# Performance work log

Measured on AMD Instinct MI355X. Metric: run time of the kernel, lower is better.

## Reference

```python
import jax, jax.numpy as jnp
import numpy as np

N = 100000   # nodes
E = 1600000  # edges (before self-loops)
F = 128      # num_features
H = 128      # hidden_dim
EPS = 1e-5   # BatchNorm eps


def setup_inputs() -> dict:
    key = jax.random.key(0)
    ks = jax.random.split(key, 8)
    x = jax.random.normal(ks[0], (N, F), dtype=jnp.float32)
    edge_index = jax.random.randint(ks[1], (2, E), 0, N, dtype=jnp.int64)

    def lin(k, din, dout):
        s = 1.0 / np.sqrt(din)
        kw, kb = jax.random.split(k)
        W = jax.random.uniform(kw, (din, dout), jnp.float32, -s, s)
        b = jax.random.uniform(kb, (dout,), jnp.float32, -s, s)
        return W, b

    W1, b1 = lin(ks[2], F, H)
    W2, b2 = lin(ks[3], H, H)
    W3, b3 = lin(ks[4], H, H)
    Wc, bc = lin(ks[5], H, 2)

    def bn_params():
        return (jnp.ones((H,), jnp.float32), jnp.zeros((H,), jnp.float32),
                jnp.zeros((H,), jnp.float32), jnp.ones((H,), jnp.float32))

    g1, be1, rm1, rv1 = bn_params()
    g2, be2, rm2, rv2 = bn_params()
    g3, be3, rm3, rv3 = bn_params()

    return {"x": x, "edge_index": edge_index,
            "W1": W1, "b1": b1, "W2": W2, "b2": b2, "W3": W3, "b3": b3,
            "g1": g1, "be1": be1, "rm1": rm1, "rv1": rv1,
            "g2": g2, "be2": be2, "rm2": rm2, "rv2": rv2,
            "g3": g3, "be3": be3, "rm3": rm3, "rv3": rv3,
            "Wc": Wc, "bc": bc}


def _gcn_norm(edge_index, num_nodes):
    # add self-loops, compute symmetric normalization (PyG GCNConv default)
    loop = jnp.arange(num_nodes, dtype=edge_index.dtype)
    src = jnp.concatenate([edge_index[0], loop])
    dst = jnp.concatenate([edge_index[1], loop])
    deg = jax.ops.segment_sum(jnp.ones_like(dst, dtype=jnp.float32), dst,
                              num_segments=num_nodes)
    dinv = jnp.where(deg > 0, jax.lax.rsqrt(deg), 0.0)
    norm = dinv[src] * dinv[dst]  # [E+N]
    return src, dst, norm


def _gcn_conv(x, W, b, src, dst, norm, num_nodes):
    h = x @ W                              # [N, H] linear first
    msg = h[src] * norm[:, None]           # gather + scale  [E+N, H]
    out = jax.ops.segment_sum(msg, dst, num_segments=num_nodes)  # scatter-add
    return out + b


def _bn_eval(x, g, be, rm, rv):
    return (x - rm) * jax.lax.rsqrt(rv + EPS) * g + be


def reference(x, edge_index,
              W1, b1, W2, b2, W3, b3,
              g1, be1, rm1, rv1,
              g2, be2, rm2, rv2,
              g3, be3, rm3, rv3,
              Wc, bc):
    n = x.shape[0]
    src, dst, norm = _gcn_norm(edge_index, n)
    h = _gcn_conv(x, W1, b1, src, dst, norm, n)
    h = _bn_eval(jax.nn.relu(h), g1, be1, rm1, rv1)
    # dropout: identity in eval mode
    h = _gcn_conv(h, W2, b2, src, dst, norm, n)
    h = _bn_eval(jax.nn.relu(h), g2, be2, rm2, rv2)
    h = _gcn_conv(h, W3, b3, src, dst, norm, n)
    h = _bn_eval(jax.nn.relu(h), g3, be3, rm3, rv3)
    return h @ Wc + bc  # [N, 2]
```

## Files before the change

kernel.cpp:

```cpp
#include <hip/hip_runtime.h>
#include <hip/hip_fp16.h>

#define BN_EPS 1e-5f
#define CHUNK 4096
#define BBITS 7

typedef _Float16 half8 __attribute__((ext_vector_type(8)));
typedef float f32x4 __attribute__((ext_vector_type(4)));

__device__ __forceinline__ float4 f4zero() { return make_float4(0.f, 0.f, 0.f, 0.f); }


__global__ __launch_bounds__(256) void k_pack_hist(const float* __restrict__ W1,
                                                   const float* __restrict__ W2,
                                                   const float* __restrict__ W3,
                                                   _Float16* __restrict__ pW,
                                                   const int* __restrict__ dst,
                                                   int* __restrict__ tableT,
                                                   int nA, int nbuck, int e) {
    __shared__ int h[1024];
    int tid = threadIdx.x;
    if (blockIdx.x < 24) {
        int t = blockIdx.x * 256 + tid;
        int wi = t >> 11;
        int tt = t & 2047;
        const float* W = (wi == 0) ? W1 : ((wi == 1) ? W2 : W3);
        int kc = tt >> 9;
        int rem = tt & 511;
        int ct = rem >> 6;
        int lane = rem & 63;
        int q = lane >> 4;
        int col = ct * 16 + (lane & 15);
        half8 hh;
#pragma unroll
        for (int j = 0; j < 8; ++j)
            hh[j] = (_Float16)W[(kc * 32 + q * 8 + j) * 128 + col];
        *(half8*)(pW + (size_t)t * 8) = hh;
        return;
    }
    int blk = blockIdx.x - 24;
    for (int k = tid; k < 1024; k += 256) h[k] = 0;
    __syncthreads();
    int base = blk * CHUNK;
    if (base + CHUNK <= e && (e & 3) == 0) {
        const int4* d4 = (const int4*)(dst + base);
#pragma unroll
        for (int t = 0; t < CHUNK / 1024; ++t) {
            int4 d = d4[t * 256 + tid];
            atomicAdd(&h[d.x >> BBITS], 1);
            atomicAdd(&h[d.y >> BBITS], 1);
            atomicAdd(&h[d.z >> BBITS], 1);
            atomicAdd(&h[d.w >> BBITS], 1);
        }
    } else {
        for (int i = base + tid; i < e && i < base + CHUNK; i += 256)
            atomicAdd(&h[dst[i] >> BBITS], 1);
    }
    __syncthreads();
    for (int k = tid; k < nbuck; k += 256)
        tableT[(size_t)k * nA + blk] = h[k];
}


__global__ __launch_bounds__(1024) void k_scan_block(const int* __restrict__ in,
                                                     int* __restrict__ outp,
                                                     int* __restrict__ partials, int len) {
    __shared__ int s[1024];
    int t = threadIdx.x;
    int gid = blockIdx.x * 1024 + t;
    int v = (gid < len) ? in[gid] : 0;
    int x = v;
    s[t] = x;
    __syncthreads();
    for (int d = 1; d < 1024; d <<= 1) {
        int y = (t >= d) ? s[t - d] : 0;
        __syncthreads();
        x += y;
        s[t] = x;
        __syncthreads();
    }
    if (gid < len) outp[gid] = x - v;
    if (t == 1023) partials[blockIdx.x] = x;
}

__global__ __launch_bounds__(256) void k_scan_addp(int* __restrict__ data,
                                                   const int* __restrict__ partials, int len) {
    __shared__ int red[256];
    int tid = threadIdx.x;
    int K = blockIdx.x >> 2;
    int s = 0;
    for (int t = tid; t < K; t += 256) s += partials[t];
    red[tid] = s;
    __syncthreads();
    for (int d = 128; d > 0; d >>= 1) {
        if (tid < d) red[tid] += red[tid + d];
        __syncthreads();
    }
    int gid = blockIdx.x * 256 + tid;
    if (gid < len) data[gid] += red[0];
}


__global__ __launch_bounds__(256) void k_bucket_scatter(const int* __restrict__ src,
                                                        const int* __restrict__ dst,
                                                        const int* __restrict__ tableT,
                                                        int2* __restrict__ bed,
                                                        int nA, int nbuck, int e) {
    __shared__ int cur[1024];
    int blk = blockIdx.x, tid = threadIdx.x;
    for (int k = tid; k < nbuck; k += 256)
        cur[k] = tableT[(size_t)k * nA + blk];
    __syncthreads();
    int base = blk * CHUNK;
    if (base + CHUNK <= e && (e & 3) == 0) {
        const int4* s4 = (const int4*)(src + base);
        const int4* d4 = (const int4*)(dst + base);
#pragma unroll
        for (int t = 0; t < CHUNK / 1024; ++t) {
            int4 s = s4[t * 256 + tid];
            int4 d = d4[t * 256 + tid];
            int p0 = atomicAdd(&cur[d.x >> BBITS], 1); bed[p0] = make_int2(s.x, d.x);
            int p1 = atomicAdd(&cur[d.y >> BBITS], 1); bed[p1] = make_int2(s.y, d.y);
            int p2 = atomicAdd(&cur[d.z >> BBITS], 1); bed[p2] = make_int2(s.z, d.z);
            int p3 = atomicAdd(&cur[d.w >> BBITS], 1); bed[p3] = make_int2(s.w, d.w);
        }
    } else {
        for (int i = base + tid; i < e && i < base + CHUNK; i += 256) {
            int d = dst[i];
            int p = atomicAdd(&cur[d >> BBITS], 1);
            bed[p] = make_int2(src[i], d);
        }
    }
}


__global__ __launch_bounds__(256) void k_bucket_rank(const int2* __restrict__ bed,
                                                     const int* __restrict__ tableT,
                                                     int* __restrict__ brank,
                                                     int* __restrict__ counts,
                                                     float* __restrict__ dinv,
                                                     int* __restrict__ localOff,
                                                     int* __restrict__ btot,
                                                     int nA, int nbuck, int n, int e) {
    __shared__ int lcnt[128];
    __shared__ int lscan[128];
    int b = blockIdx.x, tid = threadIdx.x;
    if (tid < 128) lcnt[tid] = 0;
    __syncthreads();
    int start = tableT[(size_t)b * nA];
    int end = (b + 1 < nbuck) ? tableT[(size_t)(b + 1) * nA] : e;
    for (int i = start + tid; i < end; i += 256) {
        int2 q = bed[i];
        brank[i] = atomicAdd(&lcnt[q.y & 127], 1);
    }
    __syncthreads();
    int padded = 0;
    if (tid < 128) {
        padded = (lcnt[tid] + 7) & ~7;
        lscan[tid] = padded;
    }
    __syncthreads();
    for (int d = 1; d < 128; d <<= 1) {
        int y = (tid < 128 && tid >= d) ? lscan[tid - d] : 0;
        __syncthreads();
        if (tid < 128) lscan[tid] += y;
        __syncthreads();
    }
    if (tid < 128) {
        int node = (b << BBITS) + tid;
        if (node < n) {
            int c = lcnt[tid];
            counts[node] = c;
            dinv[node] = rsqrtf((float)(c + 1));
            localOff[node] = lscan[tid] - padded;
        }
        if (tid == 127) btot[b] = lscan[127];
    }
}


__global__ __launch_bounds__(1024) void k_scan_buckets(const int* __restrict__ btot,
                                                       int* __restrict__ bucketBase, int nbuck) {
    __shared__ int s[1024];
    int t = threadIdx.x;
    int v = (t < nbuck) ? btot[t] : 0;
    int x = v;
    s[t] = x;
    __syncthreads();
    for (int d = 1; d < 1024; d <<= 1) {
        int y = (t >= d) ? s[t - d] : 0;
        __syncthreads();
        x += y;
        s[t] = x;
        __syncthreads();
    }
    if (t < nbuck) bucketBase[t] = x - v;
    if (t == nbuck - 1) bucketBase[nbuck] = x;
}


__global__ __launch_bounds__(256) void k_finalize(const int* __restrict__ counts,
                                                  const int* __restrict__ localOff,
                                                  const int* __restrict__ bucketBase,
                                                  int* __restrict__ offs,
                                                  int* __restrict__ er,
                                                  const int2* __restrict__ bed,
                                                  const int* __restrict__ brank,
                                                  unsigned int* __restrict__ bufAzero,
                                                  int n, int e, int gN, int nbuck) {
    int tid = threadIdx.x;
    if (blockIdx.x < gN) {
        int node = blockIdx.x * 256 + tid;
        if (node < n) {
            int c = counts[node];
            int o = bucketBase[node >> BBITS] + localOff[node];
            offs[node] = o;
            int pc = (c + 7) & ~7;
            for (int j = c; j < pc; ++j) er[o + j] = n;
        }
        if (node == 0) offs[n] = bucketBase[nbuck];
        if (blockIdx.x == 0 && tid < 64) bufAzero[tid] = 0u;
    } else {
        int i = ((blockIdx.x - gN) * 256 + tid) * 2;
        if (i + 1 < e) {
            int4 q = *(const int4*)(bed + i);
            int2 r = *(const int2*)(brank + i);
            er[bucketBase[q.y >> BBITS] + localOff[q.y] + r.x] = q.x;
            er[bucketBase[q.w >> BBITS] + localOff[q.w] + r.y] = q.z;
        } else if (i < e) {
            int2 q = bed[i];
            er[bucketBase[q.y >> BBITS] + localOff[q.y] + brank[i]] = q.x;
        }
    }
}


template <bool AF32>
__global__ __launch_bounds__(256) void k_gemm_mfma(const void* __restrict__ Av,
                                                   const _Float16* __restrict__ pW,
                                                   const float* __restrict__ dinv,
                                                   uint4* __restrict__ C, int n) {
    __shared__ char smem[32768];
    uint4* sW = (uint4*)smem;
    int tid = threadIdx.x;

    {
        const uint4* gW = (const uint4*)pW;
#pragma unroll
        for (int i = 0; i < 8; ++i) sW[tid + 256 * i] = gW[tid + 256 * i];
    }
    __syncthreads();

    int wave = tid >> 6, lane = tid & 63;
    int quad = lane >> 4, l16 = lane & 15;
    int row0 = blockIdx.x * 64 + wave * 16;
    int arow = row0 + l16;
    int arowc = (arow < n) ? arow : (n - 1);

    half8 af[4];
    if (AF32) {
        const float* A = (const float*)Av + (size_t)arowc * 128 + quad * 8;
#pragma unroll
        for (int kc = 0; kc < 4; ++kc) {
            float4 lo = *(const float4*)(A + kc * 32);
            float4 hi = *(const float4*)(A + kc * 32 + 4);
            half8 h;
            h[0] = (_Float16)lo.x; h[1] = (_Float16)lo.y;
            h[2] = (_Float16)lo.z; h[3] = (_Float16)lo.w;
            h[4] = (_Float16)hi.x; h[5] = (_Float16)hi.y;
            h[6] = (_Float16)hi.z; h[7] = (_Float16)hi.w;
            af[kc] = h;
        }
    } else {
        const _Float16* A = (const _Float16*)Av + (size_t)arowc * 128 + quad * 8;
#pragma unroll
        for (int kc = 0; kc < 4; ++kc)
            af[kc] = *(const half8*)(A + kc * 32);
    }

    f32x4 acc[8];
#pragma unroll
    for (int ct = 0; ct < 8; ++ct) acc[ct] = (f32x4){0.f, 0.f, 0.f, 0.f};

#pragma unroll
    for (int kc = 0; kc < 4; ++kc) {
#pragma unroll
        for (int ct = 0; ct < 8; ++ct) {
            half8 bf = *(half8*)&sW[(kc * 8 + ct) * 64 + lane];
            acc[ct] = __builtin_amdgcn_mfma_f32_16x16x32_f16(af[kc], bf, acc[ct], 0, 0, 0);
        }
    }

    __syncthreads();

    _Float16* eb = (_Float16*)smem + wave * 16 * 136;
    float dv[4];
#pragma unroll
    for (int r = 0; r < 4; ++r) {
        int rr = row0 + quad * 4 + r;
        dv[r] = dinv[(rr < n) ? rr : (n - 1)];
    }
#pragma unroll
    for (int ct = 0; ct < 8; ++ct)
#pragma unroll
        for (int r = 0; r < 4; ++r)
            eb[(quad * 4 + r) * 136 + ct * 16 + l16] = (_Float16)(acc[ct][r] * dv[r]);

#pragma unroll
    for (int i = 0; i < 4; ++i) {
        int linear = i * 64 + lane;
        int r = linear >> 4, c = linear & 15;
        uint4 v = *(uint4*)((char*)eb + r * 272 + c * 16);
        int row = row0 + r;
        if (row < n) C[(size_t)row * 16 + c] = v;
    }
}


__device__ __forceinline__ void acc_row(float4& acc, uint2 q) {
    float2 f01 = __half22float2(*(__half2*)&q.x);
    float2 f23 = __half22float2(*(__half2*)&q.y);
    acc.x += f01.x; acc.y += f01.y; acc.z += f23.x; acc.w += f23.y;
}

template <bool FUSE_CLS>
__global__ __launch_bounds__(256) void k_aggregate(const uint2* __restrict__ Ah,
                                                   const int* __restrict__ offs,
                                                   const int* __restrict__ er,
                                                   const float* __restrict__ dinv,
                                                   const float* __restrict__ bias,
                                                   const float* __restrict__ g,
                                                   const float* __restrict__ be,
                                                   const float* __restrict__ rm,
                                                   const float* __restrict__ rv,
                                                   uint2* __restrict__ Hout,
                                                   const float* __restrict__ Wc,
                                                   const float* __restrict__ bc,
                                                   float* __restrict__ out, int n) {
    int lane = threadIdx.x & 31;
    int node = blockIdx.x * 8 + (threadIdx.x >> 5);
    if (node >= n) return;

    float4 acc = f4zero();
    acc_row(acc, Ah[(size_t)node * 32 + lane]);

    int e0 = offs[node], e1 = offs[node + 1];
    for (int e = e0; e < e1; e += 8) {
        int4 ra = *(const int4*)(er + e);
        int4 rb = *(const int4*)(er + e + 4);
        uint2 v0 = Ah[(size_t)ra.x * 32 + lane];
        uint2 v1 = Ah[(size_t)ra.y * 32 + lane];
        uint2 v2 = Ah[(size_t)ra.z * 32 + lane];
        uint2 v3 = Ah[(size_t)ra.w * 32 + lane];
        uint2 v4 = Ah[(size_t)rb.x * 32 + lane];
        uint2 v5 = Ah[(size_t)rb.y * 32 + lane];
        uint2 v6 = Ah[(size_t)rb.z * 32 + lane];
        uint2 v7 = Ah[(size_t)rb.w * 32 + lane];
        acc_row(acc, v0); acc_row(acc, v1); acc_row(acc, v2); acc_row(acc, v3);
        acc_row(acc, v4); acc_row(acc, v5); acc_row(acc, v6); acc_row(acc, v7);
    }

    float di = dinv[node];
    acc.x *= di; acc.y *= di; acc.z *= di; acc.w *= di;

    float4 b4  = ((const float4*)bias)[lane];
    float4 g4  = ((const float4*)g)[lane];
    float4 be4 = ((const float4*)be)[lane];
    float4 rm4 = ((const float4*)rm)[lane];
    float4 rv4 = ((const float4*)rv)[lane];

    float4 o;
    float v;
    v = fmaxf(acc.x + b4.x, 0.f); o.x = (v - rm4.x) * rsqrtf(rv4.x + BN_EPS) * g4.x + be4.x;
    v = fmaxf(acc.y + b4.y, 0.f); o.y = (v - rm4.y) * rsqrtf(rv4.y + BN_EPS) * g4.y + be4.y;
    v = fmaxf(acc.z + b4.z, 0.f); o.z = (v - rm4.z) * rsqrtf(rv4.z + BN_EPS) * g4.z + be4.z;
    v = fmaxf(acc.w + b4.w, 0.f); o.w = (v - rm4.w) * rsqrtf(rv4.w + BN_EPS) * g4.w + be4.w;

    if (!FUSE_CLS) {
        __half2 p0 = __floats2half2_rn(o.x, o.y);
        __half2 p1 = __floats2half2_rn(o.z, o.w);
        uint2 u;
        u.x = *(unsigned int*)&p0;
        u.y = *(unsigned int*)&p1;
        Hout[(size_t)node * 32 + lane] = u;
    } else {
        const float4* Wv = (const float4*)Wc;
        float4 w01 = Wv[2 * lane];
        float4 w23 = Wv[2 * lane + 1];
        float p0 = o.x * w01.x + o.y * w01.z + o.z * w23.x + o.w * w23.z;
        float p1 = o.x * w01.y + o.y * w01.w + o.z * w23.y + o.w * w23.w;
#pragma unroll
        for (int d = 16; d >= 1; d >>= 1) {
            p0 += __shfl_down(p0, d, 32);
            p1 += __shfl_down(p1, d, 32);
        }
        if (lane == 0) {
            out[node * 2 + 0] = p0 + bc[0];
            out[node * 2 + 1] = p1 + bc[1];
        }
    }
}


extern "C" void kernel_launch(void* const* d_in, const int* in_sizes, int n_in,
                              void* d_out, int out_size, void* d_ws, size_t ws_size,
                              hipStream_t stream) {
    const float* x   = (const float*)d_in[0];
    const int*   ei  = (const int*)d_in[1];
    const float* W1  = (const float*)d_in[2];
    const float* b1  = (const float*)d_in[3];
    const float* W2  = (const float*)d_in[4];
    const float* b2  = (const float*)d_in[5];
    const float* W3  = (const float*)d_in[6];
    const float* b3  = (const float*)d_in[7];
    const float* g1  = (const float*)d_in[8];
    const float* be1 = (const float*)d_in[9];
    const float* rm1 = (const float*)d_in[10];
    const float* rv1 = (const float*)d_in[11];
    const float* g2  = (const float*)d_in[12];
    const float* be2 = (const float*)d_in[13];
    const float* rm2 = (const float*)d_in[14];
    const float* rv2 = (const float*)d_in[15];
    const float* g3  = (const float*)d_in[16];
    const float* be3 = (const float*)d_in[17];
    const float* rm3 = (const float*)d_in[18];
    const float* rv3 = (const float*)d_in[19];
    const float* Wc  = (const float*)d_in[20];
    const float* bc  = (const float*)d_in[21];
    float* out = (float*)d_out;

    int n = in_sizes[0] / 128;
    int e = in_sizes[1] / 2;
    const int* src = ei;
    const int* dst = ei + e;

    char* ws = (char*)d_ws;
    size_t off = 0;
    auto alloc = [&](size_t bytes) -> char* {
        char* p = ws + off;
        off += (bytes + 255) & ~(size_t)255;
        return p;
    };
    int nA    = (e + CHUNK - 1) / CHUNK;
    int nbuck = (n + (1 << BBITS) - 1) >> BBITS;
    int tlen  = nbuck * nA;
    int erCap = e + 8 * n;

    char*      bufA     = (char*) alloc((size_t)(n + 1) * 256);
    char*      bufH     = (char*) alloc((size_t)n * 256);
    float*     dinv     = (float*)alloc((size_t)n * 4);
    int*       counts   = (int*)  alloc((size_t)n * 4);
    int*       offs     = (int*)  alloc((size_t)(n + 1) * 4);
    int*       localOff = (int*)  alloc((size_t)n * 4);
    int*       btot     = (int*)  alloc((size_t)(nbuck + 1) * 4);
    int*       bktBase  = (int*)  alloc((size_t)(nbuck + 1) * 4);
    int*       tableT   = (int*)  alloc((size_t)(tlen + 1) * 4);
    int*       parts    = (int*)  alloc(8192);
    int*       er       = (int*)  alloc((size_t)erCap * 4);
    _Float16*  pW       = (_Float16*)alloc(3 * 16384 * 2);
    (void)ws_size; (void)n_in; (void)out_size;

    int2* bed   = (int2*)bufH;
    int*  brank = (int*)(bufH + (size_t)e * 8);

    int gN  = (n + 255) / 256;
    int nbT = (tlen + 1023) / 1024;

    k_pack_hist<<<24 + nA, 256, 0, stream>>>(W1, W2, W3, pW, dst, tableT, nA, nbuck, e);
    k_scan_block<<<nbT, 1024, 0, stream>>>(tableT, tableT, parts, tlen);
    k_scan_addp<<<(tlen + 255) / 256, 256, 0, stream>>>(tableT, parts, tlen);
    k_bucket_scatter<<<nA, 256, 0, stream>>>(src, dst, tableT, bed, nA, nbuck, e);
    k_bucket_rank<<<nbuck, 256, 0, stream>>>(bed, tableT, brank, counts, dinv, localOff,
                                             btot, nA, nbuck, n, e);
    k_scan_buckets<<<1, 1024, 0, stream>>>(btot, bktBase, nbuck);
    int gP = gN + (e / 2 + 255) / 256 + 1;
    k_finalize<<<gP, 256, 0, stream>>>(counts, localOff, bktBase, offs, er, bed, brank,
                                       (unsigned int*)(bufA + (size_t)n * 256), n, e, gN, nbuck);

    int gGemm = (n + 63) / 64;
    int gAgg  = (n + 7) / 8;

    k_gemm_mfma<true><<<gGemm, 256, 0, stream>>>(x, pW, dinv, (uint4*)bufA, n);
    k_aggregate<false><<<gAgg, 256, 0, stream>>>((const uint2*)bufA, offs, er, dinv,
                                                 b1, g1, be1, rm1, rv1, (uint2*)bufH,
                                                 nullptr, nullptr, nullptr, n);

    k_gemm_mfma<false><<<gGemm, 256, 0, stream>>>(bufH, pW + 16384, dinv, (uint4*)bufA, n);
    k_aggregate<false><<<gAgg, 256, 0, stream>>>((const uint2*)bufA, offs, er, dinv,
                                                 b2, g2, be2, rm2, rv2, (uint2*)bufH,
                                                 nullptr, nullptr, nullptr, n);

    k_gemm_mfma<false><<<gGemm, 256, 0, stream>>>(bufH, pW + 32768, dinv, (uint4*)bufA, n);
    k_aggregate<true><<<gAgg, 256, 0, stream>>>((const uint2*)bufA, offs, er, dinv,
                                                b3, g3, be3, rm3, rv3, nullptr,
                                                Wc, bc, out, n);
}
```

Measured before the change: 394.7 us.

## Fuse CSR preprocessing kernels into one cooperative persistent kernel with grid syncs

Replaces seven separate preprocessing launches (weight pack and histogram, two-level scan, bucket scatter, bucket rank, bucket scan, finalize) with one cooperative kernel of 512 blocks that loops over work and separates phases with grid.sync. This is meant to remove launch gaps and tail effects between the small preprocessing kernels. The cost is that each phase is limited to a fixed grid with grid-stride loops, and each of the seven grid barriers adds its own overhead. The old alignment check ((e & 3) == 0) on the vectorized path is also dropped.

```diff
diff --git a/kernel.cpp b/kernel.cpp
--- a/kernel.cpp
+++ b/kernel.cpp
@@ -1,9 +1,13 @@
 #include <hip/hip_runtime.h>
 #include <hip/hip_fp16.h>
+#include <hip/hip_cooperative_groups.h>
+
+namespace cg = cooperative_groups;
 
 #define BN_EPS 1e-5f
 #define CHUNK 4096
 #define BBITS 7
+#define PREP_G 512
 
 typedef _Float16 half8 __attribute__((ext_vector_type(8)));
 typedef float f32x4 __attribute__((ext_vector_type(4)));
@@ -11,20 +15,35 @@
 __device__ __forceinline__ float4 f4zero() { return make_float4(0.f, 0.f, 0.f, 0.f); }
 
 
-__global__ __launch_bounds__(256) void k_pack_hist(const float* __restrict__ W1,
-                                                   const float* __restrict__ W2,
-                                                   const float* __restrict__ W3,
-                                                   _Float16* __restrict__ pW,
-                                                   const int* __restrict__ dst,
-                                                   int* __restrict__ tableT,
-                                                   int nA, int nbuck, int e) {
-    __shared__ int h[1024];
-    int tid = threadIdx.x;
-    if (blockIdx.x < 24) {
-        int t = blockIdx.x * 256 + tid;
+struct PrepArgs {
+    const float* W1; const float* W2; const float* W3;
+    _Float16* pW;
+    const int* src; const int* dst;
+    int* tableT;
+    int* parts;
+    int2* bed;
+    int* brank;
+    int* counts;
+    float* dinv;
+    int* localOff;
+    int* btot;
+    int* bucketBase;
+    int* offs;
+    int* er;
+    unsigned int* bufAzero;
+    int nA, nbuck, tlen, nseg, n, e;
+};
+
+__global__ __launch_bounds__(256) void k_prep(PrepArgs P) {
+    cg::grid_group grid = cg::this_grid();
+    __shared__ int smem[1280];
+    int bid = blockIdx.x, tid = threadIdx.x;
+    int G = gridDim.x;
+
+    for (int t = bid * 256 + tid; t < 6144; t += G * 256) {
         int wi = t >> 11;
         int tt = t & 2047;
-        const float* W = (wi == 0) ? W1 : ((wi == 1) ? W2 : W3);
+        const float* W = (wi == 0) ? P.W1 : ((wi == 1) ? P.W2 : P.W3);
         int kc = tt >> 9;
         int rem = tt & 511;
         int ct = rem >> 6;
@@ -35,201 +54,211 @@
 #pragma unroll
         for (int j = 0; j < 8; ++j)
             hh[j] = (_Float16)W[(kc * 32 + q * 8 + j) * 128 + col];
-        *(half8*)(pW + (size_t)t * 8) = hh;
-        return;
-    }
-    int blk = blockIdx.x - 24;
-    for (int k = tid; k < 1024; k += 256) h[k] = 0;
-    __syncthreads();
-    int base = blk * CHUNK;
-    if (base + CHUNK <= e && (e & 3) == 0) {
-        const int4* d4 = (const int4*)(dst + base);
-#pragma unroll
-        for (int t = 0; t < CHUNK / 1024; ++t) {
-            int4 d = d4[t * 256 + tid];
-            atomicAdd(&h[d.x >> BBITS], 1);
-            atomicAdd(&h[d.y >> BBITS], 1);
-            atomicAdd(&h[d.z >> BBITS], 1);
-            atomicAdd(&h[d.w >> BBITS], 1);
-        }
-    } else {
-        for (int i = base + tid; i < e && i < base + CHUNK; i += 256)
-            atomicAdd(&h[dst[i] >> BBITS], 1);
-    }
-    __syncthreads();
-    for (int k = tid; k < nbuck; k += 256)
-        tableT[(size_t)k * nA + blk] = h[k];
-}
-
-
-__global__ __launch_bounds__(1024) void k_scan_block(const int* __restrict__ in,
-                                                     int* __restrict__ outp,
-                                                     int* __restrict__ partials, int len) {
-    __shared__ int s[1024];
-    int t = threadIdx.x;
-    int gid = blockIdx.x * 1024 + t;
-    int v = (gid < len) ? in[gid] : 0;
-    int x = v;
-    s[t] = x;
-    __syncthreads();
-    for (int d = 1; d < 1024; d <<= 1) {
-        int y = (t >= d) ? s[t - d] : 0;
-        __syncthreads();
-        x += y;
-        s[t] = x;
-        __syncthreads();
-    }
-    if (gid < len) outp[gid] = x - v;
-    if (t == 1023) partials[blockIdx.x] = x;
-}
-
-__global__ __launch_bounds__(256) void k_scan_addp(int* __restrict__ data,
-                                                   const int* __restrict__ partials, int len) {
-    __shared__ int red[256];
-    int tid = threadIdx.x;
-    int K = blockIdx.x >> 2;
-    int s = 0;
-    for (int t = tid; t < K; t += 256) s += partials[t];
-    red[tid] = s;
-    __syncthreads();
-    for (int d = 128; d > 0; d >>= 1) {
-        if (tid < d) red[tid] += red[tid + d];
-        __syncthreads();
-    }
-    int gid = blockIdx.x * 256 + tid;
-    if (gid < len) data[gid] += red[0];
-}
-
-
-__global__ __launch_bounds__(256) void k_bucket_scatter(const int* __restrict__ src,
-                                                        const int* __restrict__ dst,
-                                                        const int* __restrict__ tableT,
-                                                        int2* __restrict__ bed,
-                                                        int nA, int nbuck, int e) {
-    __shared__ int cur[1024];
-    int blk = blockIdx.x, tid = threadIdx.x;
-    for (int k = tid; k < nbuck; k += 256)
-        cur[k] = tableT[(size_t)k * nA + blk];
-    __syncthreads();
-    int base = blk * CHUNK;
-    if (base + CHUNK <= e && (e & 3) == 0) {
-        const int4* s4 = (const int4*)(src + base);
-        const int4* d4 = (const int4*)(dst + base);
-#pragma unroll
-        for (int t = 0; t < CHUNK / 1024; ++t) {
-            int4 s = s4[t * 256 + tid];
-            int4 d = d4[t * 256 + tid];
-            int p0 = atomicAdd(&cur[d.x >> BBITS], 1); bed[p0] = make_int2(s.x, d.x);
-            int p1 = atomicAdd(&cur[d.y >> BBITS], 1); bed[p1] = make_int2(s.y, d.y);
-            int p2 = atomicAdd(&cur[d.z >> BBITS], 1); bed[p2] = make_int2(s.z, d.z);
-            int p3 = atomicAdd(&cur[d.w >> BBITS], 1); bed[p3] = make_int2(s.w, d.w);
-        }
-    } else {
-        for (int i = base + tid; i < e && i < base + CHUNK; i += 256) {
-            int d = dst[i];
-            int p = atomicAdd(&cur[d >> BBITS], 1);
-            bed[p] = make_int2(src[i], d);
-        }
-    }
-}
-
-
-__global__ __launch_bounds__(256) void k_bucket_rank(const int2* __restrict__ bed,
-                                                     const int* __restrict__ tableT,
-                                                     int* __restrict__ brank,
-                                                     int* __restrict__ counts,
-                                                     float* __restrict__ dinv,
-                                                     int* __restrict__ localOff,
-                                                     int* __restrict__ btot,
-                                                     int nA, int nbuck, int n, int e) {
-    __shared__ int lcnt[128];
-    __shared__ int lscan[128];
-    int b = blockIdx.x, tid = threadIdx.x;
-    if (tid < 128) lcnt[tid] = 0;
-    __syncthreads();
-    int start = tableT[(size_t)b * nA];
-    int end = (b + 1 < nbuck) ? tableT[(size_t)(b + 1) * nA] : e;
-    for (int i = start + tid; i < end; i += 256) {
-        int2 q = bed[i];
-        brank[i] = atomicAdd(&lcnt[q.y & 127], 1);
-    }
-    __syncthreads();
-    int padded = 0;
-    if (tid < 128) {
-        padded = (lcnt[tid] + 7) & ~7;
-        lscan[tid] = padded;
-    }
-    __syncthreads();
-    for (int d = 1; d < 128; d <<= 1) {
-        int y = (tid < 128 && tid >= d) ? lscan[tid - d] : 0;
-        __syncthreads();
-        if (tid < 128) lscan[tid] += y;
-        __syncthreads();
-    }
-    if (tid < 128) {
-        int node = (b << BBITS) + tid;
-        if (node < n) {
-            int c = lcnt[tid];
-            counts[node] = c;
-            dinv[node] = rsqrtf((float)(c + 1));
-            localOff[node] = lscan[tid] - padded;
-        }
-        if (tid == 127) btot[b] = lscan[127];
-    }
-}
-
-
-__global__ __launch_bounds__(1024) void k_scan_buckets(const int* __restrict__ btot,
-                                                       int* __restrict__ bucketBase, int nbuck) {
-    __shared__ int s[1024];
-    int t = threadIdx.x;
-    int v = (t < nbuck) ? btot[t] : 0;
-    int x = v;
-    s[t] = x;
-    __syncthreads();
-    for (int d = 1; d < 1024; d <<= 1) {
-        int y = (t >= d) ? s[t - d] : 0;
-        __syncthreads();
-        x += y;
-        s[t] = x;
-        __syncthreads();
-    }
-    if (t < nbuck) bucketBase[t] = x - v;
-    if (t == nbuck - 1) bucketBase[nbuck] = x;
-}
-
-
-__global__ __launch_bounds__(256) void k_finalize(const int* __restrict__ counts,
-                                                  const int* __restrict__ localOff,
-                                                  const int* __restrict__ bucketBase,
-                                                  int* __restrict__ offs,
-                                                  int* __restrict__ er,
-                                                  const int2* __restrict__ bed,
-                                                  const int* __restrict__ brank,
-                                                  unsigned int* __restrict__ bufAzero,
-                                                  int n, int e, int gN, int nbuck) {
-    int tid = threadIdx.x;
-    if (blockIdx.x < gN) {
-        int node = blockIdx.x * 256 + tid;
-        if (node < n) {
-            int c = counts[node];
-            int o = bucketBase[node >> BBITS] + localOff[node];
-            offs[node] = o;
-            int pc = (c + 7) & ~7;
-            for (int j = c; j < pc; ++j) er[o + j] = n;
-        }
-        if (node == 0) offs[n] = bucketBase[nbuck];
-        if (blockIdx.x == 0 && tid < 64) bufAzero[tid] = 0u;
-    } else {
-        int i = ((blockIdx.x - gN) * 256 + tid) * 2;
-        if (i + 1 < e) {
-            int4 q = *(const int4*)(bed + i);
-            int2 r = *(const int2*)(brank + i);
-            er[bucketBase[q.y >> BBITS] + localOff[q.y] + r.x] = q.x;
-            er[bucketBase[q.w >> BBITS] + localOff[q.w] + r.y] = q.z;
-        } else if (i < e) {
-            int2 q = bed[i];
-            er[bucketBase[q.y >> BBITS] + localOff[q.y] + brank[i]] = q.x;
+        *(half8*)(P.pW + (size_t)t * 8) = hh;
+    }
+    for (int c = bid; c < P.nA; c += G) {
+        for (int k = tid; k < 1024; k += 256) smem[k] = 0;
+        __syncthreads();
+        int base = c * CHUNK;
+        if (base + CHUNK <= P.e) {
+            const int4* d4 = (const int4*)(P.dst + base);
+#pragma unroll
+            for (int t = 0; t < CHUNK / 1024; ++t) {
+                int4 d = d4[t * 256 + tid];
+                atomicAdd(&smem[d.x >> BBITS], 1);
+                atomicAdd(&smem[d.y >> BBITS], 1);
+                atomicAdd(&smem[d.z >> BBITS], 1);
+                atomicAdd(&smem[d.w >> BBITS], 1);
+            }
+        } else {
+            for (int i = base + tid; i < P.e; i += 256)
+                atomicAdd(&smem[P.dst[i] >> BBITS], 1);
+        }
+        __syncthreads();
+        for (int k = tid; k < P.nbuck; k += 256)
+            P.tableT[(size_t)k * P.nA + c] = smem[k];
+        __syncthreads();
+    }
+    grid.sync();
+
+    for (int s = bid; s < P.nseg; s += G) {
+        int base = s * 1024;
+        int v[4], loc[4], tsum = 0;
+#pragma unroll
+        for (int j = 0; j < 4; ++j) {
+            int idx = base + tid * 4 + j;
+            v[j] = (idx < P.tlen) ? P.tableT[idx] : 0;
+            loc[j] = tsum;
+            tsum += v[j];
+        }
+        int x = tsum;
+        smem[tid] = x;
+        __syncthreads();
+        for (int d = 1; d < 256; d <<= 1) {
+            int y = (tid >= d) ? smem[tid - d] : 0;
+            __syncthreads();
+            x += y;
+            smem[tid] = x;
+            __syncthreads();
+        }
+        int excl = x - tsum;
+#pragma unroll
+        for (int j = 0; j < 4; ++j) {
+            int idx = base + tid * 4 + j;
+            if (idx < P.tlen) P.tableT[idx] = excl + loc[j];
+        }
+        if (tid == 255) P.parts[s] = excl + tsum;
+        __syncthreads();
+    }
+    grid.sync();
+
+    if (bid == 0) {
+        int v[4], loc[4], tsum = 0;
+#pragma unroll
+        for (int j = 0; j < 4; ++j) {
+            int idx = tid * 4 + j;
+            v[j] = (idx < P.nseg) ? P.parts[idx] : 0;
+            loc[j] = tsum;
+            tsum += v[j];
+        }
+        int x = tsum;
+        smem[tid] = x;
+        __syncthreads();
+        for (int d = 1; d < 256; d <<= 1) {
+            int y = (tid >= d) ? smem[tid - d] : 0;
+            __syncthreads();
+            x += y;
+            smem[tid] = x;
+            __syncthreads();
+        }
+        int excl = x - tsum;
+#pragma unroll
+        for (int j = 0; j < 4; ++j) {
+            int idx = tid * 4 + j;
+            if (idx < P.nseg) P.parts[idx] = excl + loc[j];
+        }
+    }
+    grid.sync();
+
+    for (int i = bid * 256 + tid; i < P.tlen; i += G * 256)
+        P.tableT[i] += P.parts[i >> 10];
+    grid.sync();
+
+    for (int c = bid; c < P.nA; c += G) {
+        for (int k = tid; k < P.nbuck; k += 256)
+            smem[k] = P.tableT[(size_t)k * P.nA + c];
+        __syncthreads();
+        int base = c * CHUNK;
+        if (base + CHUNK <= P.e) {
+            const int4* s4 = (const int4*)(P.src + base);
+            const int4* d4 = (const int4*)(P.dst + base);
+#pragma unroll
+            for (int t = 0; t < CHUNK / 1024; ++t) {
+                int4 s = s4[t * 256 + tid];
+                int4 d = d4[t * 256 + tid];
+                int p0 = atomicAdd(&smem[d.x >> BBITS], 1); P.bed[p0] = make_int2(s.x, d.x);
+                int p1 = atomicAdd(&smem[d.y >> BBITS], 1); P.bed[p1] = make_int2(s.y, d.y);
+                int p2 = atomicAdd(&smem[d.z >> BBITS], 1); P.bed[p2] = make_int2(s.z, d.z);
+                int p3 = atomicAdd(&smem[d.w >> BBITS], 1); P.bed[p3] = make_int2(s.w, d.w);
+            }
+        } else {
+            for (int i = base + tid; i < P.e; i += 256) {
+                int d = P.dst[i];
+                int p = atomicAdd(&smem[d >> BBITS], 1);
+                P.bed[p] = make_int2(P.src[i], d);
+            }
+        }
+        __syncthreads();
+    }
+    grid.sync();
+
+    for (int b = bid; b < P.nbuck; b += G) {
+        int* lcnt = smem;
+        int* lscan = smem + 128;
+        if (tid < 128) lcnt[tid] = 0;
+        __syncthreads();
+        int start = P.tableT[(size_t)b * P.nA];
+        int end = (b + 1 < P.nbuck) ? P.tableT[(size_t)(b + 1) * P.nA] : P.e;
+        for (int i = start + tid; i < end; i += 256) {
+            int2 q = P.bed[i];
+            P.brank[i] = atomicAdd(&lcnt[q.y & 127], 1);
+        }
+        __syncthreads();
+        int padded = 0;
+        if (tid < 128) {
+            padded = (lcnt[tid] + 7) & ~7;
+            lscan[tid] = padded;
+        }
+        __syncthreads();
+        for (int d = 1; d < 128; d <<= 1) {
+            int y = (tid < 128 && tid >= d) ? lscan[tid - d] : 0;
+            __syncthreads();
+            if (tid < 128) lscan[tid] += y;
+            __syncthreads();
+        }
+        if (tid < 128) {
+            int node = (b << BBITS) + tid;
+            if (node < P.n) {
+                int c = lcnt[tid];
+                P.counts[node] = c;
+                P.dinv[node] = rsqrtf((float)(c + 1));
+                P.localOff[node] = lscan[tid] - padded;
+            }
+            if (tid == 127) P.btot[b] = lscan[127];
+        }
+        __syncthreads();
+    }
+    grid.sync();
+
+    if (bid == 0) {
+        int v[4], loc[4], tsum = 0;
+#pragma unroll
+        for (int j = 0; j < 4; ++j) {
+            int idx = tid * 4 + j;
+            v[j] = (idx < P.nbuck) ? P.btot[idx] : 0;
+            loc[j] = tsum;
+            tsum += v[j];
+        }
+        int x = tsum;
+        smem[tid] = x;
+        __syncthreads();
+        for (int d = 1; d < 256; d <<= 1) {
+            int y = (tid >= d) ? smem[tid - d] : 0;
+            __syncthreads();
+            x += y;
+            smem[tid] = x;
+            __syncthreads();
+        }
+        int excl = x - tsum;
+#pragma unroll
+        for (int j = 0; j < 4; ++j) {
+            int idx = tid * 4 + j;
+            if (idx < P.nbuck) P.bucketBase[idx] = excl + loc[j];
+            if (idx == P.nbuck - 1) P.bucketBase[P.nbuck] = excl + loc[j] + v[j];
+        }
+    }
+    grid.sync();
+
+    if (bid == 0 && tid < 64) P.bufAzero[tid] = 0u;
+    for (int node = bid * 256 + tid; node < P.n; node += G * 256) {
+        int c = P.counts[node];
+        int o = P.bucketBase[node >> BBITS] + P.localOff[node];
+        P.offs[node] = o;
+        int pc = (c + 7) & ~7;
+        for (int j = c; j < pc; ++j) P.er[o + j] = P.n;
+    }
+    if (bid == 0 && tid == 0) P.offs[P.n] = P.bucketBase[P.nbuck];
+    int npair = (P.e + 1) / 2;
+    for (int ip = bid * 256 + tid; ip < npair; ip += G * 256) {
+        int i = ip * 2;
+        if (i + 1 < P.e) {
+            int4 q = *(const int4*)(P.bed + i);
+            int2 r = *(const int2*)(P.brank + i);
+            P.er[P.bucketBase[q.y >> BBITS] + P.localOff[q.y] + r.x] = q.x;
+            P.er[P.bucketBase[q.w >> BBITS] + P.localOff[q.w] + r.y] = q.z;
+        } else {
+            int2 q = P.bed[i];
+            P.er[P.bucketBase[q.y >> BBITS] + P.localOff[q.y] + P.brank[i]] = q.x;
         }
     }
 }
@@ -444,6 +473,7 @@
     int nA    = (e + CHUNK - 1) / CHUNK;
     int nbuck = (n + (1 << BBITS) - 1) >> BBITS;
     int tlen  = nbuck * nA;
+    int nseg  = (tlen + 1023) / 1024;
     int erCap = e + 8 * n;
 
     char*      bufA     = (char*) alloc((size_t)(n + 1) * 256);
@@ -455,7 +485,7 @@
     int*       btot     = (int*)  alloc((size_t)(nbuck + 1) * 4);
     int*       bktBase  = (int*)  alloc((size_t)(nbuck + 1) * 4);
     int*       tableT   = (int*)  alloc((size_t)(tlen + 1) * 4);
-    int*       parts    = (int*)  alloc(8192);
+    int*       parts    = (int*)  alloc((size_t)(nseg + 1) * 4);
     int*       er       = (int*)  alloc((size_t)erCap * 4);
     _Float16*  pW       = (_Float16*)alloc(3 * 16384 * 2);
     (void)ws_size; (void)n_in; (void)out_size;
@@ -463,19 +493,21 @@
     int2* bed   = (int2*)bufH;
     int*  brank = (int*)(bufH + (size_t)e * 8);
 
-    int gN  = (n + 255) / 256;
-    int nbT = (tlen + 1023) / 1024;
-
-    k_pack_hist<<<24 + nA, 256, 0, stream>>>(W1, W2, W3, pW, dst, tableT, nA, nbuck, e);
-    k_scan_block<<<nbT, 1024, 0, stream>>>(tableT, tableT, parts, tlen);
-    k_scan_addp<<<(tlen + 255) / 256, 256, 0, stream>>>(tableT, parts, tlen);
-    k_bucket_scatter<<<nA, 256, 0, stream>>>(src, dst, tableT, bed, nA, nbuck, e);
-    k_bucket_rank<<<nbuck, 256, 0, stream>>>(bed, tableT, brank, counts, dinv, localOff,
-                                             btot, nA, nbuck, n, e);
-    k_scan_buckets<<<1, 1024, 0, stream>>>(btot, bktBase, nbuck);
-    int gP = gN + (e / 2 + 255) / 256 + 1;
-    k_finalize<<<gP, 256, 0, stream>>>(counts, localOff, bktBase, offs, er, bed, brank,
-                                       (unsigned int*)(bufA + (size_t)n * 256), n, e, gN, nbuck);
+    PrepArgs pa;
+    pa.W1 = W1; pa.W2 = W2; pa.W3 = W3; pa.pW = pW;
+    pa.src = src; pa.dst = dst;
+    pa.tableT = tableT; pa.parts = parts;
+    pa.bed = bed; pa.brank = brank;
+    pa.counts = counts; pa.dinv = dinv; pa.localOff = localOff;
+    pa.btot = btot; pa.bucketBase = bktBase;
+    pa.offs = offs; pa.er = er;
+    pa.bufAzero = (unsigned int*)(bufA + (size_t)n * 256);
+    pa.nA = nA; pa.nbuck = nbuck; pa.tlen = tlen; pa.nseg = nseg;
+    pa.n = n; pa.e = e;
+
+    void* kargs[] = { &pa };
+    hipLaunchCooperativeKernel((const void*)k_prep, dim3(PREP_G), dim3(256),
+                               kargs, 0, stream);
 
     int gGemm = (n + 63) / 64;
     int gAgg  = (n + 7) / 8;
```

Result: slower. 827.2 us (+109.6%).
